# Kernel optimization log

Measured on AMD Instinct MI355X. Metric: run time of the kernel, lower is better.

## Reference

```python
import jax, jax.numpy as jnp
import numpy as np

N, E, G, T = 4096, 16384, 128, 100
DIMS = [(5, 64), (64, 128), (128, 256)]
EPS = 1e-5


def setup_inputs() -> dict:
    key = jax.random.key(0)
    ks = iter(jax.random.split(key, 64))
    d = {}
    d["x"] = jax.random.normal(next(ks), (N, 5), jnp.float32)
    d["edge_index"] = jax.random.randint(next(ks), (2, E), 0, N, jnp.int64)
    d["edge_attr"] = jax.random.uniform(next(ks), (E, 3), jnp.float32)
    d["batch_seg"] = jnp.sort(jax.random.randint(next(ks), (N,), 0, G, jnp.int64))
    for l, (cin, cout) in enumerate(DIMS, start=1):
        d[f"l{l}_W1"] = jax.random.normal(next(ks), (3, 32), jnp.float32) * 0.3
        d[f"l{l}_b1"] = jnp.zeros((32,), jnp.float32)
        d[f"l{l}_W2"] = jax.random.normal(next(ks), (32, cin * cout), jnp.float32) * 0.05
        d[f"l{l}_b2"] = jnp.zeros((cin * cout,), jnp.float32)
        d[f"l{l}_root"] = jax.random.normal(next(ks), (cin, cout), jnp.float32) * 0.1
        d[f"l{l}_bias"] = jnp.zeros((cout,), jnp.float32)
        d[f"bn{l}_g"] = jnp.ones((cout,), jnp.float32)
        d[f"bn{l}_b"] = jnp.zeros((cout,), jnp.float32)
        d[f"bn{l}_m"] = jax.random.normal(next(ks), (cout,), jnp.float32) * 0.01
        d[f"bn{l}_v"] = jax.random.uniform(next(ks), (cout,), jnp.float32, 0.5, 1.5)
    d["mlp_W"] = jax.random.normal(next(ks), (256, T), jnp.float32) * 0.06
    d["mlp_b"] = jnp.zeros((T,), jnp.float32)
    return d


def _nnconv(h, src, dst, edge_attr, W1, b1, W2, b2, root, bias, cin, cout):
    # edge MLP -> per-edge weight matrix [E, cin, cout]
    ew = (jax.nn.relu(edge_attr @ W1 + b1) @ W2 + b2).reshape(-1, cin, cout)
    msg = jnp.einsum('ei,eio->eo', h[src], ew)  # gather + per-edge matmul
    ssum = jax.ops.segment_sum(msg, dst, num_segments=N)
    cnt = jax.ops.segment_sum(jnp.ones((msg.shape[0],), msg.dtype), dst, num_segments=N)
    agg = ssum / jnp.maximum(cnt, 1.0)[:, None]  # scatter-mean
    return h @ root + agg + bias


def _bn(h, g, b, m, v):
    return g * (h - m) * jax.lax.rsqrt(v + EPS) + b


def reference(x, edge_index, edge_attr, batch_seg,
              l1_W1, l1_b1, l1_W2, l1_b2, l1_root, l1_bias, bn1_g, bn1_b, bn1_m, bn1_v,
              l2_W1, l2_b1, l2_W2, l2_b2, l2_root, l2_bias, bn2_g, bn2_b, bn2_m, bn2_v,
              l3_W1, l3_b1, l3_W2, l3_b2, l3_root, l3_bias, bn3_g, bn3_b, bn3_m, bn3_v,
              mlp_W, mlp_b):
    src, dst = edge_index[0], edge_index[1]
    h = _nnconv(x, src, dst, edge_attr, l1_W1, l1_b1, l1_W2, l1_b2, l1_root, l1_bias, 5, 64)
    h = jax.nn.relu(_bn(h, bn1_g, bn1_b, bn1_m, bn1_v))
    h = _nnconv(h, src, dst, edge_attr, l2_W1, l2_b1, l2_W2, l2_b2, l2_root, l2_bias, 64, 128)
    h = jax.nn.relu(_bn(h, bn2_g, bn2_b, bn2_m, bn2_v))
    h = _nnconv(h, src, dst, edge_attr, l3_W1, l3_b1, l3_W2, l3_b2, l3_root, l3_bias, 128, 256)
    h = jax.nn.relu(_bn(h, bn3_g, bn3_b, bn3_m, bn3_v))
    # global mean pool over graphs
    psum = jax.ops.segment_sum(h, batch_seg, num_segments=G)
    pcnt = jax.ops.segment_sum(jnp.ones((N,), h.dtype), batch_seg, num_segments=G)
    pooled = psum / jnp.maximum(pcnt, 1.0)[:, None]
    out = pooled @ mlp_W + mlp_b
    return jnp.where(out > 0, out, 0.1 * out)  # LeakyReLU(0.1)
```

## Files before the change

kernel.cpp:

```cpp
#include <hip/hip_runtime.h>
#include <cstdint>
#include <cstddef>

#define BN_EPS 1e-5f

typedef short bf16x8 __attribute__((ext_vector_type(8)));
typedef float f32x4  __attribute__((ext_vector_type(4)));
typedef unsigned short u16x8 __attribute__((ext_vector_type(8)));

__device__ __forceinline__ uint16_t f2bf_rte(float f) {
  uint32_t u = __float_as_uint(f);
  uint32_t r = u + 0x7fffu + ((u >> 16) & 1u);
  return (uint16_t)(r >> 16);
}
__device__ __forceinline__ float bf2f(uint16_t h) {
  return __uint_as_float(((uint32_t)h) << 16);
}
__device__ __forceinline__ void split_bf(float v, uint16_t& hi, uint16_t& lo) {
  hi = f2bf_rte(v);
  lo = f2bf_rte(v - bf2f(hi));
}

__global__ void zero_i32_k(int* p, int n) {
  int i = blockIdx.x * blockDim.x + threadIdx.x;
  if (i < n) p[i] = 0;
}

__global__ void hist_k(const int* __restrict__ dst, int* __restrict__ cnt, int E) {
  int e = blockIdx.x * blockDim.x + threadIdx.x;
  if (e < E) atomicAdd(&cnt[dst[e]], 1);
}

__global__ __launch_bounds__(1024) void scan_k(const int* __restrict__ cnt,
                                               int* __restrict__ offsets,
                                               int* __restrict__ cursor,
                                               int N, int total) {
  __shared__ int part[1024];
  int t = threadIdx.x;
  int a0 = cnt[4*t+0], a1 = cnt[4*t+1], a2 = cnt[4*t+2], a3 = cnt[4*t+3];
  part[t] = a0 + a1 + a2 + a3;
  __syncthreads();
  for (int off = 1; off < 1024; off <<= 1) {
    int v = (t >= off) ? part[t - off] : 0;
    __syncthreads();
    part[t] += v;
    __syncthreads();
  }
  int excl = (t == 0) ? 0 : part[t-1];
  int o0 = excl, o1 = o0 + a0, o2 = o1 + a1, o3 = o2 + a2;
  offsets[4*t+0] = o0; offsets[4*t+1] = o1; offsets[4*t+2] = o2; offsets[4*t+3] = o3;
  cursor [4*t+0] = o0; cursor [4*t+1] = o1; cursor [4*t+2] = o2; cursor [4*t+3] = o3;
  if (t == 0) offsets[N] = total;
}

__global__ void scatter_k(const int* __restrict__ dst, int* __restrict__ cursor,
                          int* __restrict__ csr, int E) {
  int e = blockIdx.x * blockDim.x + threadIdx.x;
  if (e < E) {
    int d = dst[e];
    int pos = atomicAdd(&cursor[d], 1);
    csr[pos] = e;
  }
}

__global__ void build_W2pT_k(const float* __restrict__ W2, const float* __restrict__ b2,
                             const float* __restrict__ root,
                             uint16_t* __restrict__ Bhi, uint16_t* __restrict__ Blo,
                             int cin, int cout, int Kpad) {
  int idx = blockIdx.x * blockDim.x + threadIdx.x;
  int total = cout * Kpad;
  if (idx >= total) return;
  int o  = idx / Kpad;
  int ki = idx - o * Kpad;
  float v = 0.f;
  if (ki < 34 * cin) {
    int k = ki / cin;
    int i = ki - k * cin;
    if (k < 32)       v = W2[(size_t)k * cin * cout + (size_t)i * cout + o];
    else if (k == 32) v = b2[(size_t)i * cout + o];
    else              v = root[(size_t)i * cout + o];
  }
  uint16_t hi, lo;
  split_bf(v, hi, lo);
  Bhi[idx] = hi;
  Blo[idx] = lo;
}

template<int CIN>
__global__ __launch_bounds__(256) void build_S_vec_k(const float* __restrict__ h,
                                                     const float* __restrict__ ea,
                                                     const float* __restrict__ W1,
                                                     const float* __restrict__ b1,
                                                     const int* __restrict__ src,
                                                     const int* __restrict__ csr,
                                                     const int* __restrict__ offsets,
                                                     uint16_t* __restrict__ Shi,
                                                     uint16_t* __restrict__ Slo,
                                                     int Kpad) {
  constexpr int CH = 8;
  constexpr int K1 = 33 * CIN;
  constexpr int NCH = K1 / 8;
  constexpr int NP = (NCH + 255) / 256;
  __shared__ float hs[CH][CIN];
  __shared__ float zs[CH][33];
  __shared__ int   es[CH];
  const int n = blockIdx.x;
  const int tid = threadIdx.x;
  const int base = offsets[n];
  const int deg  = offsets[n+1] - base;
  const float scale = 1.f / fmaxf((float)deg, 1.f);
  float acc[NP][8];
#pragma unroll
  for (int p = 0; p < NP; p++)
#pragma unroll
    for (int j = 0; j < 8; j++) acc[p][j] = 0.f;

  for (int c0 = 0; c0 < deg; c0 += CH) {
    const int cc = min(CH, deg - c0);
    if (tid < cc) es[tid] = csr[base + c0 + tid];
    __syncthreads();
    for (int idx = tid; idx < cc * CIN; idx += 256) {
      int slot = idx / CIN, i = idx - slot * CIN;
      hs[slot][i] = h[(size_t)src[es[slot]] * CIN + i];
    }
    for (int idx = tid; idx < cc * 33; idx += 256) {
      int slot = idx / 33, k = idx - slot * 33;
      float v;
      if (k == 32) v = 1.f;
      else {
        int e = es[slot];
        v = fmaxf(ea[e*3+0] * W1[k] + ea[e*3+1] * W1[32 + k] + ea[e*3+2] * W1[64 + k] + b1[k], 0.f);
      }
      zs[slot][k] = v;
    }
    __syncthreads();
#pragma unroll
    for (int p = 0; p < NP; p++) {
      int ch = p * 256 + tid;
      if (ch < NCH) {
        int ki0 = ch * 8;
        int k  = ki0 / CIN;
        int i0 = ki0 & (CIN - 1);
        for (int c = 0; c < cc; c++) {
          float zv = zs[c][k];
          float4 h0 = *(const float4*)&hs[c][i0];
          float4 h1 = *(const float4*)&hs[c][i0 + 4];
          acc[p][0] += zv * h0.x; acc[p][1] += zv * h0.y;
          acc[p][2] += zv * h0.z; acc[p][3] += zv * h0.w;
          acc[p][4] += zv * h1.x; acc[p][5] += zv * h1.y;
          acc[p][6] += zv * h1.z; acc[p][7] += zv * h1.w;
        }
      }
    }
    __syncthreads();
  }
  const size_t rowb = (size_t)n * Kpad;
#pragma unroll
  for (int p = 0; p < NP; p++) {
    int ch = p * 256 + tid;
    if (ch < NCH) {
      u16x8 hv, lv;
#pragma unroll
      for (int j = 0; j < 8; j++) {
        uint16_t hi, lo;
        split_bf(acc[p][j] * scale, hi, lo);
        hv[j] = hi; lv[j] = lo;
      }
      *(u16x8*)(Shi + rowb + ch * 8) = hv;
      *(u16x8*)(Slo + rowb + ch * 8) = lv;
    }
  }
  for (int c = tid; c < CIN / 8; c += 256) {
    int i0 = c * 8;
    float4 a = *(const float4*)&h[(size_t)n * CIN + i0];
    float4 b = *(const float4*)&h[(size_t)n * CIN + i0 + 4];
    float vals[8] = {a.x, a.y, a.z, a.w, b.x, b.y, b.z, b.w};
    u16x8 hv, lv;
#pragma unroll
    for (int j = 0; j < 8; j++) {
      uint16_t hi, lo;
      split_bf(vals[j], hi, lo);
      hv[j] = hi; lv[j] = lo;
    }
    *(u16x8*)(Shi + rowb + K1 + i0) = hv;
    *(u16x8*)(Slo + rowb + K1 + i0) = lv;
  }
  for (int ki = 34 * CIN + tid; ki < Kpad; ki += 256) {
    Shi[rowb + ki] = 0;
    Slo[rowb + ki] = 0;
  }
}

__global__ __launch_bounds__(256) void build_S5_k(const float* __restrict__ h,
                                                  const float* __restrict__ ea,
                                                  const float* __restrict__ W1,
                                                  const float* __restrict__ b1,
                                                  const int* __restrict__ src,
                                                  const int* __restrict__ csr,
                                                  const int* __restrict__ offsets,
                                                  uint16_t* __restrict__ Shi,
                                                  uint16_t* __restrict__ Slo,
                                                  int Kpad) {
  constexpr int CIN = 5, CH = 8;
  constexpr int K1 = 33 * CIN;
  constexpr int KT = 34 * CIN;
  __shared__ float hs[CH][CIN];
  __shared__ float zs[CH][33];
  __shared__ int   es[CH];
  const int n = blockIdx.x;
  const int tid = threadIdx.x;
  const int base = offsets[n];
  const int deg  = offsets[n+1] - base;
  const float scale = 1.f / fmaxf((float)deg, 1.f);
  float acc = 0.f;

  for (int c0 = 0; c0 < deg; c0 += CH) {
    const int cc = min(CH, deg - c0);
    if (tid < cc) es[tid] = csr[base + c0 + tid];
    __syncthreads();
    for (int idx = tid; idx < cc * CIN; idx += 256) {
      int slot = idx / CIN, i = idx - slot * CIN;
      hs[slot][i] = h[(size_t)src[es[slot]] * CIN + i];
    }
    for (int idx = tid; idx < cc * 33; idx += 256) {
      int slot = idx / 33, k = idx - slot * 33;
      float v;
      if (k == 32) v = 1.f;
      else {
        int e = es[slot];
        v = fmaxf(ea[e*3+0] * W1[k] + ea[e*3+1] * W1[32 + k] + ea[e*3+2] * W1[64 + k] + b1[k], 0.f);
      }
      zs[slot][k] = v;
    }
    __syncthreads();
    if (tid < K1) {
      int k = tid / CIN, i = tid - (tid / CIN) * CIN;
      float a = acc;
      for (int c = 0; c < cc; c++) a += zs[c][k] * hs[c][i];
      acc = a;
    }
    __syncthreads();
  }
  const size_t rowb = (size_t)n * Kpad;
  if (tid < K1) {
    uint16_t hi, lo;
    split_bf(acc * scale, hi, lo);
    Shi[rowb + tid] = hi;
    Slo[rowb + tid] = lo;
  }
  if (tid < CIN) {
    uint16_t hi, lo;
    split_bf(h[(size_t)n * CIN + tid], hi, lo);
    Shi[rowb + K1 + tid] = hi;
    Slo[rowb + K1 + tid] = lo;
  }
  for (int ki = KT + tid; ki < Kpad; ki += 256) {
    Shi[rowb + ki] = 0;
    Slo[rowb + ki] = 0;
  }
}

__global__ __launch_bounds__(256, 4) void mfma_gemm_sk_k(const uint16_t* __restrict__ Ahi,
                                                         const uint16_t* __restrict__ Alo,
                                                         const uint16_t* __restrict__ Bhi,
                                                         const uint16_t* __restrict__ Blo,
                                                         float* __restrict__ Cpart,
                                                         int Kpad, int Ncol, int M,
                                                         int itersPerSplit) {
  __shared__ uint16_t As[2][64][72];
  __shared__ uint16_t Bs[2][64][72];
  const int m0 = blockIdx.x * 64, n0 = blockIdx.y * 64;
  const int kbeg = blockIdx.z * itersPerSplit * 64;
  const int kend = min(Kpad, kbeg + itersPerSplit * 64);
  const int tid  = threadIdx.x;
  const int lane = tid & 63;
  const int wave = tid >> 6;
  const int wm = wave & 1, wn = wave >> 1;
  const int q  = lane >> 4;
  const int mr = lane & 15;

  f32x4 acc[2][2];
#pragma unroll
  for (int a = 0; a < 2; a++)
#pragma unroll
    for (int b = 0; b < 2; b++) acc[a][b] = (f32x4)0.f;

  for (int k0 = kbeg; k0 < kend; k0 += 64) {
#pragma unroll
    for (int rep = 0; rep < 2; rep++) {
      int chunk = rep * 256 + tid;
      int r = chunk >> 3, c = chunk & 7;
      size_t ga = (size_t)(m0 + r) * Kpad + k0 + c * 8;
      size_t gb = (size_t)(n0 + r) * Kpad + k0 + c * 8;
      *(uint4*)&As[0][r][c * 8] = *(const uint4*)(Ahi + ga);
      *(uint4*)&As[1][r][c * 8] = *(const uint4*)(Alo + ga);
      *(uint4*)&Bs[0][r][c * 8] = *(const uint4*)(Bhi + gb);
      *(uint4*)&Bs[1][r][c * 8] = *(const uint4*)(Blo + gb);
    }
    __syncthreads();
#pragma unroll
    for (int ks = 0; ks < 2; ks++) {
      const int kb = ks * 32 + q * 8;
      bf16x8 ah[2], al[2], bh[2], bl[2];
#pragma unroll
      for (int f = 0; f < 2; f++) {
        ah[f] = *(const bf16x8*)&As[0][wm * 32 + f * 16 + mr][kb];
        al[f] = *(const bf16x8*)&As[1][wm * 32 + f * 16 + mr][kb];
        bh[f] = *(const bf16x8*)&Bs[0][wn * 32 + f * 16 + mr][kb];
        bl[f] = *(const bf16x8*)&Bs[1][wn * 32 + f * 16 + mr][kb];
      }
#pragma unroll
      for (int fm = 0; fm < 2; fm++)
#pragma unroll
        for (int fn = 0; fn < 2; fn++) {
          acc[fm][fn] = __builtin_amdgcn_mfma_f32_16x16x32_bf16(ah[fm], bh[fn], acc[fm][fn], 0, 0, 0);
          acc[fm][fn] = __builtin_amdgcn_mfma_f32_16x16x32_bf16(ah[fm], bl[fn], acc[fm][fn], 0, 0, 0);
          acc[fm][fn] = __builtin_amdgcn_mfma_f32_16x16x32_bf16(al[fm], bh[fn], acc[fm][fn], 0, 0, 0);
        }
    }
    __syncthreads();
  }

  float* Cz = Cpart + (size_t)blockIdx.z * M * Ncol;
#pragma unroll
  for (int fm = 0; fm < 2; fm++) {
#pragma unroll
    for (int reg = 0; reg < 4; reg++) {
      int row = m0 + wm * 32 + fm * 16 + q * 4 + reg;
#pragma unroll
      for (int fn = 0; fn < 2; fn++) {
        int col = n0 + wn * 32 + fn * 16 + mr;
        Cz[(size_t)row * Ncol + col] = acc[fm][fn][reg];
      }
    }
  }
}

__global__ void epilogue_k(const float* __restrict__ Cpart, int SK, size_t plane4,
                           int Ncol,
                           const float* __restrict__ bias, const float* __restrict__ bg,
                           const float* __restrict__ bb, const float* __restrict__ bnm,
                           const float* __restrict__ bnv,
                           float* __restrict__ C, int total4) {
  int i = blockIdx.x * blockDim.x + threadIdx.x;
  if (i >= total4) return;
  float4 v = {0.f, 0.f, 0.f, 0.f};
  for (int z = 0; z < SK; z++) {
    float4 p = *((const float4*)Cpart + (size_t)z * plane4 + i);
    v.x += p.x; v.y += p.y; v.z += p.z; v.w += p.w;
  }
  int col0 = (i * 4) % Ncol;
  float o[4] = {v.x, v.y, v.z, v.w};
#pragma unroll
  for (int j = 0; j < 4; j++) {
    int c = col0 + j;
    float s = bg[c] * rsqrtf(bnv[c] + BN_EPS);
    float val = (o[j] + bias[c] - bnm[c]) * s + bb[c];
    o[j] = fmaxf(val, 0.f);
  }
  float4 r = {o[0], o[1], o[2], o[3]};
  *((float4*)C + i) = r;
}

__global__ __launch_bounds__(256) void pool_final_k(const float* __restrict__ h,
                                                    const int* __restrict__ seg,
                                                    const float* __restrict__ W,
                                                    const float* __restrict__ b,
                                                    float* __restrict__ out,
                                                    int N, int T) {
  __shared__ float pooled[256];
  const int g = blockIdx.x, tid = threadIdx.x;
  int lo = 0, hi = N;
  while (lo < hi) { int mid = (lo + hi) >> 1; if (seg[mid] < g) lo = mid + 1; else hi = mid; }
  int lo2 = lo, hi2 = N;
  while (lo2 < hi2) { int mid = (lo2 + hi2) >> 1; if (seg[mid] < g + 1) lo2 = mid + 1; else hi2 = mid; }
  const int cnt = lo2 - lo;
  const float inv = 1.f / fmaxf((float)cnt, 1.f);
  float s = 0.f;
  for (int n = lo; n < lo2; n++) s += h[(size_t)n * 256 + tid];
  pooled[tid] = s * inv;
  __syncthreads();
  if (tid < T) {
    float acc = b[tid];
    for (int o = 0; o < 256; o++) acc += pooled[o] * W[(size_t)o * T + tid];
    out[(size_t)g * T + tid] = (acc > 0.f) ? acc : 0.1f * acc;
  }
}

extern "C" void kernel_launch(void* const* d_in, const int* in_sizes, int n_in,
                              void* d_out, int out_size, void* d_ws, size_t ws_size,
                              hipStream_t stream) {
  const float* x   = (const float*)d_in[0];
  const int*   ei  = (const int*)d_in[1];
  const float* ea  = (const float*)d_in[2];
  const int*   seg = (const int*)d_in[3];

  const int N = in_sizes[0] / 5;
  const int E = in_sizes[2] / 3;
  const int T = in_sizes[35];
  const int G = out_size / T;
  const int* src = ei;
  const int* dst = ei + E;

  const float *W1[3], *b1[3], *W2[3], *b2[3], *root[3], *bias[3];
  const float *bng[3], *bnb[3], *bnm[3], *bnv[3];
  for (int l = 0; l < 3; l++) {
    int base = 4 + l * 10;
    W1[l]   = (const float*)d_in[base + 0];
    b1[l]   = (const float*)d_in[base + 1];
    W2[l]   = (const float*)d_in[base + 2];
    b2[l]   = (const float*)d_in[base + 3];
    root[l] = (const float*)d_in[base + 4];
    bias[l] = (const float*)d_in[base + 5];
    bng[l]  = (const float*)d_in[base + 6];
    bnb[l]  = (const float*)d_in[base + 7];
    bnm[l]  = (const float*)d_in[base + 8];
    bnv[l]  = (const float*)d_in[base + 9];
  }
  const float* mlpW = (const float*)d_in[34];
  const float* mlpb = (const float*)d_in[35];

  char* p = (char*)d_ws;
  auto carve = [&](size_t bytes) -> char* {
    char* r = p;
    p += (bytes + 255) & ~(size_t)255;
    return r;
  };
  const int KPADMAX = 4352;
  const int SKMAX = 8;
  int*      cnt     = (int*)carve((size_t)N * 4);
  int*      offsets = (int*)carve((size_t)(N + 1) * 4);
  int*      cursor  = (int*)carve((size_t)N * 4);
  int*      csr     = (int*)carve((size_t)E * 4);
  uint16_t* Whi     = (uint16_t*)carve((size_t)256 * KPADMAX * 2);
  uint16_t* Wlo     = (uint16_t*)carve((size_t)256 * KPADMAX * 2);
  uint16_t* Shi     = (uint16_t*)carve((size_t)N * KPADMAX * 2);
  uint16_t* Slo     = (uint16_t*)carve((size_t)N * KPADMAX * 2);
  float*    Cpart   = (float*)carve((size_t)SKMAX * N * 256 * 4 / 2);
  float*    hA      = (float*)carve((size_t)N * 256 * 4);
  float*    hB      = (float*)carve((size_t)N * 128 * 4);

  zero_i32_k<<<(N + 255) / 256, 256, 0, stream>>>(cnt, N);
  hist_k<<<(E + 255) / 256, 256, 0, stream>>>(dst, cnt, E);
  scan_k<<<1, 1024, 0, stream>>>(cnt, offsets, cursor, N, E);
  scatter_k<<<(E + 255) / 256, 256, 0, stream>>>(dst, cursor, csr, E);

  const int cins[3]  = {5, 64, 128};
  const int couts[3] = {64, 128, 256};
  const int kpads[3] = {192, 2176, 4352};
  const int sks[3]   = {1, 8, 4};
  const float* hin = x;
  float* houts[3] = {hB, hB, hA};
  houts[0] = hA; houts[1] = hB; houts[2] = hA;

  for (int l = 0; l < 3; l++) {
    int cin = cins[l], cout = couts[l], Kpad = kpads[l], SK = sks[l];
    int iters = Kpad / 64;
    int ips = (iters + SK - 1) / SK;
    build_W2pT_k<<<(cout * Kpad + 255) / 256, 256, 0, stream>>>(W2[l], b2[l], root[l],
                                                                Whi, Wlo, cin, cout, Kpad);
    if (cin == 5)
      build_S5_k<<<N, 256, 0, stream>>>(hin, ea, W1[l], b1[l], src, csr, offsets, Shi, Slo, Kpad);
    else if (cin == 64)
      build_S_vec_k<64><<<N, 256, 0, stream>>>(hin, ea, W1[l], b1[l], src, csr, offsets, Shi, Slo, Kpad);
    else
      build_S_vec_k<128><<<N, 256, 0, stream>>>(hin, ea, W1[l], b1[l], src, csr, offsets, Shi, Slo, Kpad);
    dim3 grid(N / 64, cout / 64, SK);
    mfma_gemm_sk_k<<<grid, 256, 0, stream>>>(Shi, Slo, Whi, Wlo, Cpart, Kpad, cout, N, ips);
    int total4 = N * cout / 4;
    epilogue_k<<<(total4 + 255) / 256, 256, 0, stream>>>(Cpart, SK, (size_t)N * cout / 4, cout,
                                                         bias[l], bng[l], bnb[l], bnm[l], bnv[l],
                                                         houts[l], total4);
    hin = houts[l];
  }

  pool_final_k<<<G, 256, 0, stream>>>(hA, seg, mlpW, mlpb, (float*)d_out, N, T);
}
```

Before: 290.0 us.

## Enlarge split-K MFMA GEMM tiles to 128x128 with XOR-swizzled LDS

The split-K bf16x3 GEMM now uses 128x128 output tiles with 4x4 MFMA fragments per wave instead of 64x64 tiles. This raises data reuse per LDS load. The padded LDS rows are replaced by an XOR-swizzled layout to avoid bank conflicts. Split-K counts are raised and K iterations are distributed evenly across splits, with column bounds checks for the 64-wide layer. The cost is more registers and lower occupancy (launch bounds 2), a larger partial-sum buffer, and more epilogue reduction work.

```diff
diff --git a/kernel.cpp b/kernel.cpp
--- a/kernel.cpp
+++ b/kernel.cpp
@@ -260,18 +260,20 @@
   }
 }
 
-__global__ __launch_bounds__(256, 4) void mfma_gemm_sk_k(const uint16_t* __restrict__ Ahi,
-                                                         const uint16_t* __restrict__ Alo,
-                                                         const uint16_t* __restrict__ Bhi,
-                                                         const uint16_t* __restrict__ Blo,
-                                                         float* __restrict__ Cpart,
-                                                         int Kpad, int Ncol, int M,
-                                                         int itersPerSplit) {
-  __shared__ uint16_t As[2][64][72];
-  __shared__ uint16_t Bs[2][64][72];
-  const int m0 = blockIdx.x * 64, n0 = blockIdx.y * 64;
-  const int kbeg = blockIdx.z * itersPerSplit * 64;
-  const int kend = min(Kpad, kbeg + itersPerSplit * 64);
+__global__ __launch_bounds__(256, 2) void mfma_gemm_sk2_k(const uint16_t* __restrict__ Ahi,
+                                                          const uint16_t* __restrict__ Alo,
+                                                          const uint16_t* __restrict__ Bhi,
+                                                          const uint16_t* __restrict__ Blo,
+                                                          float* __restrict__ Cpart,
+                                                          int Kpad, int Ncol, int M,
+                                                          int iters, int SK) {
+  __shared__ uint16_t As[2][128][64];
+  __shared__ uint16_t Bs[2][128][64];
+  const int m0 = blockIdx.x * 128, n0 = blockIdx.y * 128;
+  const int z  = blockIdx.z;
+  const int ibase = iters / SK, irem = iters % SK;
+  const int i0    = z * ibase + min(z, irem);
+  const int niter = ibase + (z < irem ? 1 : 0);
   const int tid  = threadIdx.x;
   const int lane = tid & 63;
   const int wave = tid >> 6;
@@ -279,58 +281,68 @@
   const int q  = lane >> 4;
   const int mr = lane & 15;
 
-  f32x4 acc[2][2];
-#pragma unroll
-  for (int a = 0; a < 2; a++)
-#pragma unroll
-    for (int b = 0; b < 2; b++) acc[a][b] = (f32x4)0.f;
-
-  for (int k0 = kbeg; k0 < kend; k0 += 64) {
-#pragma unroll
-    for (int rep = 0; rep < 2; rep++) {
-      int chunk = rep * 256 + tid;
-      int r = chunk >> 3, c = chunk & 7;
-      size_t ga = (size_t)(m0 + r) * Kpad + k0 + c * 8;
-      size_t gb = (size_t)(n0 + r) * Kpad + k0 + c * 8;
-      *(uint4*)&As[0][r][c * 8] = *(const uint4*)(Ahi + ga);
-      *(uint4*)&As[1][r][c * 8] = *(const uint4*)(Alo + ga);
-      *(uint4*)&Bs[0][r][c * 8] = *(const uint4*)(Bhi + gb);
-      *(uint4*)&Bs[1][r][c * 8] = *(const uint4*)(Blo + gb);
+  f32x4 acc[4][4];
+#pragma unroll
+  for (int a = 0; a < 4; a++)
+#pragma unroll
+    for (int b = 0; b < 4; b++) acc[a][b] = (f32x4)0.f;
+
+  for (int it = 0; it < niter; it++) {
+    const int k0 = (i0 + it) * 64;
+#pragma unroll
+    for (int i = 0; i < 16; i++) {
+      int chunk = i * 256 + tid;
+      int coct = chunk & 7;
+      int row  = (chunk >> 3) & 127;
+      int plane = (chunk >> 10) & 1;
+      int arr   = chunk >> 11;
+      const uint16_t* gsrc = arr ? (plane ? Blo : Bhi) : (plane ? Alo : Ahi);
+      int grow = (arr ? n0 : m0) + row;
+      uint4 v = {0u, 0u, 0u, 0u};
+      if (arr == 0 || grow < Ncol)
+        v = *(const uint4*)(gsrc + (size_t)grow * Kpad + k0 + coct * 8);
+      int soct = coct ^ (row & 7);
+      uint16_t* ldst = arr ? &Bs[plane][row][soct * 8] : &As[plane][row][soct * 8];
+      *(uint4*)ldst = v;
     }
     __syncthreads();
 #pragma unroll
     for (int ks = 0; ks < 2; ks++) {
-      const int kb = ks * 32 + q * 8;
-      bf16x8 ah[2], al[2], bh[2], bl[2];
-#pragma unroll
-      for (int f = 0; f < 2; f++) {
-        ah[f] = *(const bf16x8*)&As[0][wm * 32 + f * 16 + mr][kb];
-        al[f] = *(const bf16x8*)&As[1][wm * 32 + f * 16 + mr][kb];
-        bh[f] = *(const bf16x8*)&Bs[0][wn * 32 + f * 16 + mr][kb];
-        bl[f] = *(const bf16x8*)&Bs[1][wn * 32 + f * 16 + mr][kb];
-      }
-#pragma unroll
-      for (int fm = 0; fm < 2; fm++)
-#pragma unroll
-        for (int fn = 0; fn < 2; fn++) {
-          acc[fm][fn] = __builtin_amdgcn_mfma_f32_16x16x32_bf16(ah[fm], bh[fn], acc[fm][fn], 0, 0, 0);
-          acc[fm][fn] = __builtin_amdgcn_mfma_f32_16x16x32_bf16(ah[fm], bl[fn], acc[fm][fn], 0, 0, 0);
-          acc[fm][fn] = __builtin_amdgcn_mfma_f32_16x16x32_bf16(al[fm], bh[fn], acc[fm][fn], 0, 0, 0);
+      const int oct = (ks * 4 + q) ^ (mr & 7);
+      bf16x8 bh[4], bl[4];
+#pragma unroll
+      for (int f = 0; f < 4; f++) {
+        int row = wn * 64 + f * 16 + mr;
+        bh[f] = *(const bf16x8*)&Bs[0][row][oct * 8];
+        bl[f] = *(const bf16x8*)&Bs[1][row][oct * 8];
+      }
+#pragma unroll
+      for (int fm = 0; fm < 4; fm++) {
+        int row = wm * 64 + fm * 16 + mr;
+        bf16x8 ah = *(const bf16x8*)&As[0][row][oct * 8];
+        bf16x8 al = *(const bf16x8*)&As[1][row][oct * 8];
+#pragma unroll
+        for (int fn = 0; fn < 4; fn++) {
+          acc[fm][fn] = __builtin_amdgcn_mfma_f32_16x16x32_bf16(ah, bh[fn], acc[fm][fn], 0, 0, 0);
+          acc[fm][fn] = __builtin_amdgcn_mfma_f32_16x16x32_bf16(ah, bl[fn], acc[fm][fn], 0, 0, 0);
+          acc[fm][fn] = __builtin_amdgcn_mfma_f32_16x16x32_bf16(al, bh[fn], acc[fm][fn], 0, 0, 0);
         }
-    }
-    __syncthreads();
-  }
-
-  float* Cz = Cpart + (size_t)blockIdx.z * M * Ncol;
-#pragma unroll
-  for (int fm = 0; fm < 2; fm++) {
+      }
+    }
+    __syncthreads();
+  }
+
+  float* Cz = Cpart + (size_t)z * M * Ncol;
+#pragma unroll
+  for (int fm = 0; fm < 4; fm++) {
 #pragma unroll
     for (int reg = 0; reg < 4; reg++) {
-      int row = m0 + wm * 32 + fm * 16 + q * 4 + reg;
-#pragma unroll
-      for (int fn = 0; fn < 2; fn++) {
-        int col = n0 + wn * 32 + fn * 16 + mr;
-        Cz[(size_t)row * Ncol + col] = acc[fm][fn][reg];
+      int row = m0 + wm * 64 + fm * 16 + q * 4 + reg;
+#pragma unroll
+      for (int fn = 0; fn < 4; fn++) {
+        int col = n0 + wn * 64 + fn * 16 + mr;
+        if (col < Ncol)
+          Cz[(size_t)row * Ncol + col] = acc[fm][fn][reg];
       }
     }
   }
@@ -427,7 +439,6 @@
     return r;
   };
   const int KPADMAX = 4352;
-  const int SKMAX = 8;
   int*      cnt     = (int*)carve((size_t)N * 4);
   int*      offsets = (int*)carve((size_t)(N + 1) * 4);
   int*      cursor  = (int*)carve((size_t)N * 4);
@@ -436,7 +447,7 @@
   uint16_t* Wlo     = (uint16_t*)carve((size_t)256 * KPADMAX * 2);
   uint16_t* Shi     = (uint16_t*)carve((size_t)N * KPADMAX * 2);
   uint16_t* Slo     = (uint16_t*)carve((size_t)N * KPADMAX * 2);
-  float*    Cpart   = (float*)carve((size_t)SKMAX * N * 256 * 4 / 2);
+  float*    Cpart   = (float*)carve((size_t)16 * N * 128 * 4);
   float*    hA      = (float*)carve((size_t)N * 256 * 4);
   float*    hB      = (float*)carve((size_t)N * 128 * 4);
 
@@ -448,15 +459,13 @@
   const int cins[3]  = {5, 64, 128};
   const int couts[3] = {64, 128, 256};
   const int kpads[3] = {192, 2176, 4352};
-  const int sks[3]   = {1, 8, 4};
+  const int sks[3]   = {3, 16, 8};
   const float* hin = x;
-  float* houts[3] = {hB, hB, hA};
-  houts[0] = hA; houts[1] = hB; houts[2] = hA;
+  float* houts[3] = {hA, hB, hA};
 
   for (int l = 0; l < 3; l++) {
     int cin = cins[l], cout = couts[l], Kpad = kpads[l], SK = sks[l];
     int iters = Kpad / 64;
-    int ips = (iters + SK - 1) / SK;
     build_W2pT_k<<<(cout * Kpad + 255) / 256, 256, 0, stream>>>(W2[l], b2[l], root[l],
                                                                 Whi, Wlo, cin, cout, Kpad);
     if (cin == 5)
@@ -465,8 +474,8 @@
       build_S_vec_k<64><<<N, 256, 0, stream>>>(hin, ea, W1[l], b1[l], src, csr, offsets, Shi, Slo, Kpad);
     else
       build_S_vec_k<128><<<N, 256, 0, stream>>>(hin, ea, W1[l], b1[l], src, csr, offsets, Shi, Slo, Kpad);
-    dim3 grid(N / 64, cout / 64, SK);
-    mfma_gemm_sk_k<<<grid, 256, 0, stream>>>(Shi, Slo, Whi, Wlo, Cpart, Kpad, cout, N, ips);
+    dim3 grid(N / 128, (cout + 127) / 128, SK);
+    mfma_gemm_sk2_k<<<grid, 256, 0, stream>>>(Shi, Slo, Whi, Wlo, Cpart, Kpad, cout, N, iters, SK);
     int total4 = N * cout / 4;
     epilogue_k<<<(total4 + 255) / 256, 256, 0, stream>>>(Cpart, SK, (size_t)N * cout / 4, cout,
                                                          bias[l], bng[l], bnb[l], bnm[l], bnv[l],
```

Result: slower. 315.2 us (+8.7%).
